# Kernel tuning notes

Hardware: AMD Instinct MI355X
Metric: run time of the kernel (lower is better)

The kernel has to match this reference:

```python
import jax, jax.numpy as jnp
import numpy as np

L, H, P = 32768, 256, 256
DT_MIN, DT_MAX = 0.001, 0.1


def setup_inputs() -> dict:
    key = jax.random.key(0)
    ks = jax.random.split(key, 7)
    signal = jax.random.normal(ks[0], (L, H), jnp.float32)
    # stable HiPPO-like init: negative real part, random imaginary part
    lam_re = -(0.1 + 0.4 * jax.random.uniform(ks[1], (P,), jnp.float32))
    lam_im = jax.random.normal(ks[2], (P,), jnp.float32)
    Lambda_ri = jnp.stack([lam_re, lam_im], axis=-1)            # (P, 2)
    B_ri = jax.random.normal(ks[3], (P, H, 2), jnp.float32) / np.float32(np.sqrt(H))
    C_ri = jax.random.normal(ks[4], (H, P, 2), jnp.float32) / np.float32(np.sqrt(P))
    D = jax.random.uniform(ks[5], (H,), jnp.float32)
    log_step = jnp.log(DT_MIN + (DT_MAX - DT_MIN) * jax.random.uniform(ks[6], (P,), jnp.float32))
    return {"signal": signal, "Lambda_ri": Lambda_ri, "B_ri": B_ri,
            "C_ri": C_ri, "D": D, "log_step": log_step}


def reference(signal, Lambda_ri, B_ri, C_ri, D, log_step):
    # --- get_BC_tilde (bcInit='dense'): B stored real (P,H,2) -> complex ---
    Lambda = jax.lax.complex(Lambda_ri[..., 0], Lambda_ri[..., 1])   # (P,)
    B_tilde = jax.lax.complex(B_ri[..., 0], B_ri[..., 1])            # (P, H)
    C_tilde = jax.lax.complex(C_ri[..., 0], C_ri[..., 1])            # (H, P)

    # --- discretize_zoh ---
    step = jnp.exp(log_step)                                          # (P,) step_scale = 1.0
    Lambda_bar = jnp.exp(Lambda * step)                               # (P,) complex
    B_bar = ((Lambda_bar - 1.0) / Lambda)[:, None] * B_tilde          # (P, H) complex

    # --- apply_ssm: Bu_elements = vmap(u -> B_bar @ u) over time ---
    Bu = signal.astype(Lambda_bar.dtype) @ B_bar.T                    # (L, P) complex
    Lam = jnp.broadcast_to(Lambda_bar, Bu.shape)                      # (L, P)

    def binop(qi, qj):
        A_i, Bu_i = qi
        A_j, Bu_j = qj
        return (A_j * A_i, Bu_j + A_j * Bu_i)

    _, xs = jax.lax.associative_scan(binop, (Lam, Bu), axis=0)        # (L, P)

    # y = Re(C_tilde @ x) + D * u, vectorized over time
    y = jnp.real(xs @ C_tilde.T) + D * signal                         # (L, H)
    return y
```

## Files before the change

kernel.cpp:

```cpp
#include <hip/hip_runtime.h>
#include <math.h>

constexpr int L = 32768;
constexpr int H = 256;
constexpr int P = 256;
constexpr int T = 64;
constexpr int NC = L / T;
constexpr int N1 = 2 * P;
constexpr int LDE = 132;

typedef __attribute__((ext_vector_type(8))) short short8;
typedef __attribute__((ext_vector_type(4))) float f32x4;

__device__ __forceinline__ unsigned f2bf(float f) {
  unsigned u = __float_as_uint(f);
  return (u + 0x7FFFu + ((u >> 16) & 1u)) >> 16;
}
__device__ __forceinline__ float bf_lo(unsigned u) { return __uint_as_float(u << 16); }
__device__ __forceinline__ float bf_hi(unsigned u) { return __uint_as_float(u & 0xFFFF0000u); }

__device__ __forceinline__ void gload_lds16(const unsigned short* g, unsigned short* l) {
  __builtin_amdgcn_global_load_lds(
      (const __attribute__((address_space(1))) unsigned int*)(g),
      (__attribute__((address_space(3))) unsigned int*)(l), 16, 0, 0);
}

__device__ __forceinline__ void lambda_bar_of(const float* __restrict__ lam,
                                              const float* __restrict__ lstep,
                                              int p, float& lbr, float& lbi) {
  float lr = lam[2 * p], li = lam[2 * p + 1];
  float st = expf(lstep[p]);
  float ea = expf(lr * st);
  lbr = ea * cosf(li * st);
  lbi = ea * sinf(li * st);
}

__global__ __launch_bounds__(256) void k_prep(const float* __restrict__ lam,
                                              const float* __restrict__ lstep,
                                              const float* __restrict__ Bri,
                                              const float* __restrict__ Cri,
                                              unsigned short* __restrict__ Bcat,
                                              unsigned short* __restrict__ Ccat,
                                              float* __restrict__ powr,
                                              float* __restrict__ powi) {
  int idx = blockIdx.x * 256 + threadIdx.x;
  if (idx < N1 * H) {
    int n = idx >> 8, k = idx & 255;
    int p = n >> 1, comp = n & 1;
    float lr = lam[2 * p], li = lam[2 * p + 1];
    float st = expf(lstep[p]);
    float ea = expf(lr * st);
    float lbr = ea * cosf(li * st), lbi = ea * sinf(li * st);
    float inv = 1.0f / (lr * lr + li * li);
    float nr = lbr - 1.0f;
    float fr = (nr * lr + lbi * li) * inv;
    float fi = (lbi * lr - nr * li) * inv;
    float br = Bri[2 * (p * H + k)], bi = Bri[2 * (p * H + k) + 1];
    float v = (comp == 0) ? (fr * br - fi * bi) : (fr * bi + fi * br);
    Bcat[idx] = (unsigned short)f2bf(v);
  } else if (idx < 2 * N1 * H) {
    int j = idx - N1 * H;
    int h = j >> 9, k2 = j & 511;
    int p = k2 >> 1;
    float v = ((k2 & 1) == 0) ? Cri[2 * (h * P + p)] : -Cri[2 * (h * P + p) + 1];
    Ccat[j] = (unsigned short)f2bf(v);
  } else {
    int r = idx - 2 * N1 * H;
    int t = r >> 8, p = r & 255;
    float lr = lam[2 * p], li = lam[2 * p + 1];
    float st = expf(lstep[p]);
    float e = (float)(t + 1);
    float er = expf(e * lr * st);
    powr[r] = er * cosf(e * li * st);
    powi[r] = er * sinf(e * li * st);
  }
}

__global__ __launch_bounds__(256) void k_gemm1s(const float* __restrict__ sig,
                                                const unsigned short* __restrict__ Bcat,
                                                const float* __restrict__ lam,
                                                const float* __restrict__ lstep,
                                                unsigned short* __restrict__ Xl,
                                                float* __restrict__ Sr,
                                                float* __restrict__ Si) {
  constexpr int K = 256;
  __shared__ __align__(16) float sEpi[128 * LDE];
  unsigned short* sA = (unsigned short*)sEpi;
  unsigned short* sB = sA + 128 * 32;
  const int tid = threadIdx.x;
  const int lane = tid & 63;
  const int wave = tid >> 6;
  const int wr = (wave >> 1) * 64, wc = (wave & 1) * 64;
  const int m0 = blockIdx.x * 128, n0 = blockIdx.y * 128;
  const int r0 = tid >> 2;
  const int q0 = (tid & 3) * 8;
  const int frow = lane & 15, fk = (lane >> 4) * 8;
  f32x4 acc[4][4];
#pragma unroll
  for (int i = 0; i < 4; i++)
#pragma unroll
    for (int j = 0; j < 4; j++) acc[i][j] = (f32x4){0.f, 0.f, 0.f, 0.f};

  for (int k0 = 0; k0 < K; k0 += 32) {
    float4 a[2][2];
#pragma unroll
    for (int u = 0; u < 2; u++) {
      int row = r0 + u * 64;
      const float* src = sig + (size_t)(m0 + row) * K + k0 + q0;
      a[u][0] = *(const float4*)(src);
      a[u][1] = *(const float4*)(src + 4);
    }
    if (k0) __syncthreads();
    gload_lds16(Bcat + (size_t)(n0 + r0) * K + k0 + q0, sB + tid * 8);
    gload_lds16(Bcat + (size_t)(n0 + 64 + r0) * K + k0 + q0, sB + 2048 + tid * 8);
#pragma unroll
    for (int u = 0; u < 2; u++) {
      int row = r0 + u * 64;
      uint4 w;
      w.x = f2bf(a[u][0].x) | (f2bf(a[u][0].y) << 16);
      w.y = f2bf(a[u][0].z) | (f2bf(a[u][0].w) << 16);
      w.z = f2bf(a[u][1].x) | (f2bf(a[u][1].y) << 16);
      w.w = f2bf(a[u][1].z) | (f2bf(a[u][1].w) << 16);
      *(uint4*)(sA + row * 32 + q0) = w;
    }
    __syncthreads();
    short8 af[4], bfr[4];
#pragma unroll
    for (int i = 0; i < 4; i++) af[i] = *(const short8*)(sA + (wr + i * 16 + frow) * 32 + fk);
#pragma unroll
    for (int j = 0; j < 4; j++) bfr[j] = *(const short8*)(sB + (wc + j * 16 + frow) * 32 + fk);
#pragma unroll
    for (int i = 0; i < 4; i++)
#pragma unroll
      for (int j = 0; j < 4; j++)
        acc[i][j] = __builtin_amdgcn_mfma_f32_16x16x32_bf16(af[i], bfr[j], acc[i][j], 0, 0, 0);
  }

  __syncthreads();
  const int crow = wr + (lane >> 4) * 4, ccol = wc + (lane & 15);
#pragma unroll
  for (int i = 0; i < 4; i++)
#pragma unroll
    for (int j = 0; j < 4; j++)
#pragma unroll
      for (int g = 0; g < 4; g++)
        sEpi[(crow + i * 16 + g) * LDE + ccol + j * 16] = acc[i][j][g];
  __syncthreads();

  if (tid < 128) {
    const int pl = tid & 63;
    const int half = tid >> 6;
    const int c = blockIdx.x * 2 + half;
    const int gp = (n0 >> 1) + pl;
    float lbr, lbi;
    lambda_bar_of(lam, lstep, gp, lbr, lbi);
    float xr = 0.f, xi = 0.f;
    const float* e = sEpi + (half * 64) * LDE + 2 * pl;
    const size_t gbase = (size_t)(m0 + half * 64) * N1 + n0 + 2 * pl;
    for (int tb = 0; tb < T; tb += 8) {
      float2 v[8];
#pragma unroll
      for (int u = 0; u < 8; u++) v[u] = *(const float2*)(e + (tb + u) * LDE);
      unsigned ov[8];
#pragma unroll
      for (int u = 0; u < 8; u++) {
        float nr = fmaf(lbr, xr, fmaf(-lbi, xi, v[u].x));
        float ni = fmaf(lbr, xi, fmaf(lbi, xr, v[u].y));
        xr = nr; xi = ni;
        ov[u] = f2bf(xr) | (f2bf(xi) << 16);
      }
#pragma unroll
      for (int u = 0; u < 8; u++)
        *(unsigned*)(Xl + gbase + (size_t)(tb + u) * N1) = ov[u];
    }
    Sr[c * P + gp] = xr;
    Si[c * P + gp] = xi;
  }
}

__global__ __launch_bounds__(256) void k_carry(const float* __restrict__ lam,
                                               const float* __restrict__ lstep,
                                               const float* __restrict__ Sr,
                                               const float* __restrict__ Si,
                                               float* __restrict__ car, float* __restrict__ cai) {
  const int p = threadIdx.x;
  float lr = lam[2 * p], li = lam[2 * p + 1];
  float st = expf(lstep[p]);
  float ea = expf((float)T * lr * st);
  float lTr = ea * cosf((float)T * li * st);
  float lTi = ea * sinf((float)T * li * st);
  float cr = 0.f, ci = 0.f;
  for (int c0 = 0; c0 < NC; c0 += 16) {
    float vr[16], vi[16];
#pragma unroll
    for (int u = 0; u < 16; u++) {
      vr[u] = Sr[(c0 + u) * P + p];
      vi[u] = Si[(c0 + u) * P + p];
    }
#pragma unroll
    for (int u = 0; u < 16; u++) {
      car[(c0 + u) * P + p] = cr;
      cai[(c0 + u) * P + p] = ci;
      float nr = fmaf(lTr, cr, fmaf(-lTi, ci, vr[u]));
      float ni = fmaf(lTr, ci, fmaf(lTi, cr, vi[u]));
      cr = nr; ci = ni;
    }
  }
}

__global__ __launch_bounds__(256) void k_gemm2f(const unsigned short* __restrict__ Xl,
                                                const unsigned short* __restrict__ Ccat,
                                                const float* __restrict__ powr,
                                                const float* __restrict__ powi,
                                                const float* __restrict__ car,
                                                const float* __restrict__ cai,
                                                const float* __restrict__ sig,
                                                const float* __restrict__ Dv,
                                                float* __restrict__ out) {
  constexpr int K = 512;
  __shared__ __align__(16) unsigned short sA[128 * 32];
  __shared__ __align__(16) unsigned short sB[128 * 32];
  const int tid = threadIdx.x;
  const int lane = tid & 63;
  const int wave = tid >> 6;
  const int wr = (wave >> 1) * 64, wc = (wave & 1) * 64;
  const int m0 = blockIdx.x * 128, n0 = blockIdx.y * 128;
  const int bx2 = blockIdx.x * 2;
  const int r0 = tid >> 2;
  const int q0 = (tid & 3) * 8;
  const int frow = lane & 15, fk = (lane >> 4) * 8;
  f32x4 acc[4][4];
#pragma unroll
  for (int i = 0; i < 4; i++)
#pragma unroll
    for (int j = 0; j < 4; j++) acc[i][j] = (f32x4){0.f, 0.f, 0.f, 0.f};

  for (int k0 = 0; k0 < K; k0 += 32) {
    uint4 xa[2];
    float4 pr4[2], pi4[2], cr4[2], ci4[2];
#pragma unroll
    for (int u = 0; u < 2; u++) {
      int row = r0 + u * 64;
      int t = row & 63;
      int c = bx2 + (row >> 6);
      int p0 = (k0 + q0) >> 1;
      xa[u] = *(const uint4*)(Xl + (size_t)(m0 + row) * K + k0 + q0);
      pr4[u] = *(const float4*)(powr + t * P + p0);
      pi4[u] = *(const float4*)(powi + t * P + p0);
      cr4[u] = *(const float4*)(car + c * P + p0);
      ci4[u] = *(const float4*)(cai + c * P + p0);
    }
    if (k0) __syncthreads();
    gload_lds16(Ccat + (size_t)(n0 + r0) * K + k0 + q0, sB + tid * 8);
    gload_lds16(Ccat + (size_t)(n0 + 64 + r0) * K + k0 + q0, sB + 2048 + tid * 8);
#pragma unroll
    for (int u = 0; u < 2; u++) {
      int row = r0 + u * 64;
      float pr[4] = {pr4[u].x, pr4[u].y, pr4[u].z, pr4[u].w};
      float pi_[4] = {pi4[u].x, pi4[u].y, pi4[u].z, pi4[u].w};
      float cr[4] = {cr4[u].x, cr4[u].y, cr4[u].z, cr4[u].w};
      float ci_[4] = {ci4[u].x, ci4[u].y, ci4[u].z, ci4[u].w};
      unsigned xw[4] = {xa[u].x, xa[u].y, xa[u].z, xa[u].w};
      uint4 w;
      unsigned wo[4];
#pragma unroll
      for (int j = 0; j < 4; j++) {
        float xgr = bf_lo(xw[j]) + (pr[j] * cr[j] - pi_[j] * ci_[j]);
        float xgi = bf_hi(xw[j]) + (pr[j] * ci_[j] + pi_[j] * cr[j]);
        wo[j] = f2bf(xgr) | (f2bf(xgi) << 16);
      }
      w.x = wo[0]; w.y = wo[1]; w.z = wo[2]; w.w = wo[3];
      *(uint4*)(sA + row * 32 + q0) = w;
    }
    __syncthreads();
    short8 af[4], bfr[4];
#pragma unroll
    for (int i = 0; i < 4; i++) af[i] = *(const short8*)(sA + (wr + i * 16 + frow) * 32 + fk);
#pragma unroll
    for (int j = 0; j < 4; j++) bfr[j] = *(const short8*)(sB + (wc + j * 16 + frow) * 32 + fk);
#pragma unroll
    for (int i = 0; i < 4; i++)
#pragma unroll
      for (int j = 0; j < 4; j++)
        acc[i][j] = __builtin_amdgcn_mfma_f32_16x16x32_bf16(af[i], bfr[j], acc[i][j], 0, 0, 0);
  }

  const int crow = wr + (lane >> 4) * 4, ccol = wc + (lane & 15);
  float dcol[4];
#pragma unroll
  for (int j = 0; j < 4; j++) dcol[j] = Dv[n0 + ccol + j * 16];
#pragma unroll
  for (int i = 0; i < 4; i++)
#pragma unroll
    for (int j = 0; j < 4; j++) {
      int col = n0 + ccol + j * 16;
#pragma unroll
      for (int g = 0; g < 4; g++) {
        int row = m0 + crow + i * 16 + g;
        out[(size_t)row * H + col] = acc[i][j][g] + dcol[j] * sig[(size_t)row * H + col];
      }
    }
}

extern "C" void kernel_launch(void* const* d_in, const int* in_sizes, int n_in,
                              void* d_out, int out_size, void* d_ws, size_t ws_size,
                              hipStream_t stream) {
  const float* sig = (const float*)d_in[0];
  const float* lam = (const float*)d_in[1];
  const float* Bri = (const float*)d_in[2];
  const float* Cri = (const float*)d_in[3];
  const float* Dv  = (const float*)d_in[4];
  const float* lst = (const float*)d_in[5];
  float* out = (float*)d_out;

  unsigned short* Bcat = (unsigned short*)d_ws;
  unsigned short* Ccat = Bcat + (size_t)N1 * H;
  unsigned short* Xl   = Ccat + (size_t)H * N1;
  float* powr = (float*)(Xl + (size_t)L * N1);
  float* powi = powr + T * P;
  float* Sr   = powi + T * P;
  float* Si   = Sr + NC * P;
  float* car  = Si + NC * P;
  float* cai  = car + NC * P;

  k_prep<<<(2 * N1 * H + T * P) / 256, 256, 0, stream>>>(lam, lst, Bri, Cri,
                                                         Bcat, Ccat, powr, powi);
  dim3 g1(L / 128, N1 / 128);
  k_gemm1s<<<g1, 256, 0, stream>>>(sig, Bcat, lam, lst, Xl, Sr, Si);
  k_carry<<<1, 256, 0, stream>>>(lam, lst, Sr, Si, car, cai);
  dim3 g2(L / 128, H / 128);
  k_gemm2f<<<g2, 256, 0, stream>>>(Xl, Ccat, powr, powi, car, cai, sig, Dv, out);
}
```

Before: 175.0 us.

## Double-buffer both GEMM main loops and parallelize chunk carry scan across blocks

Both GEMM kernels now use double-buffered LDS tiles. The next A tile is converted and the next B tile is issued through global_load_lds while MFMAs run on the current buffers. The A tile also gets a padded stride (40) to cut LDS bank conflicts. In the first GEMM, the scan epilogue is staged in two 64-row halves so the LDS footprint shrinks. The serial single-block 512-step carry recurrence becomes a per-state block that uses a wave-level shuffle scan with precomputed Lambda^(8T) powers, removing a long latency-bound serial pass. The trade-offs are more registers for prefetched tiles and slightly different floating-point ordering in the carry.

After: 153.8 us. 1.14x faster.

```diff
diff --git a/kernel.cpp b/kernel.cpp
--- a/kernel.cpp
+++ b/kernel.cpp
@@ -7,7 +7,8 @@
 constexpr int T = 64;
 constexpr int NC = L / T;
 constexpr int N1 = 2 * P;
-constexpr int LDE = 132;
+constexpr int LDA = 40;
+constexpr int LDEP = 130;
 
 typedef __attribute__((ext_vector_type(8))) short short8;
 typedef __attribute__((ext_vector_type(4))) float f32x4;
@@ -83,17 +84,18 @@
                                                 unsigned short* __restrict__ Xl,
                                                 float* __restrict__ Sr,
                                                 float* __restrict__ Si) {
-  constexpr int K = 256;
-  __shared__ __align__(16) float sEpi[128 * LDE];
-  unsigned short* sA = (unsigned short*)sEpi;
-  unsigned short* sB = sA + 128 * 32;
+  constexpr int K = 256, NIT = K / 32;
+  __shared__ __align__(16) char smem[36864];
+  unsigned short* sA[2] = {(unsigned short*)smem, (unsigned short*)smem + 5120};
+  unsigned short* sB[2] = {(unsigned short*)smem + 10240, (unsigned short*)smem + 14336};
+  float* sEpi = (float*)smem;
   const int tid = threadIdx.x;
   const int lane = tid & 63;
   const int wave = tid >> 6;
   const int wr = (wave >> 1) * 64, wc = (wave & 1) * 64;
   const int m0 = blockIdx.x * 128, n0 = blockIdx.y * 128;
-  const int r0 = tid >> 2;
-  const int q0 = (tid & 3) * 8;
+  const int ar = tid >> 1, aq = (tid & 1) * 16;
+  const int br = tid >> 2, bq = (tid & 3) * 8;
   const int frow = lane & 15, fk = (lane >> 4) * 8;
   f32x4 acc[4][4];
 #pragma unroll
@@ -101,110 +103,144 @@
 #pragma unroll
     for (int j = 0; j < 4; j++) acc[i][j] = (f32x4){0.f, 0.f, 0.f, 0.f};
 
-  for (int k0 = 0; k0 < K; k0 += 32) {
-    float4 a[2][2];
-#pragma unroll
-    for (int u = 0; u < 2; u++) {
-      int row = r0 + u * 64;
-      const float* src = sig + (size_t)(m0 + row) * K + k0 + q0;
-      a[u][0] = *(const float4*)(src);
-      a[u][1] = *(const float4*)(src + 4);
-    }
-    if (k0) __syncthreads();
-    gload_lds16(Bcat + (size_t)(n0 + r0) * K + k0 + q0, sB + tid * 8);
-    gload_lds16(Bcat + (size_t)(n0 + 64 + r0) * K + k0 + q0, sB + 2048 + tid * 8);
-#pragma unroll
-    for (int u = 0; u < 2; u++) {
-      int row = r0 + u * 64;
-      uint4 w;
-      w.x = f2bf(a[u][0].x) | (f2bf(a[u][0].y) << 16);
-      w.y = f2bf(a[u][0].z) | (f2bf(a[u][0].w) << 16);
-      w.z = f2bf(a[u][1].x) | (f2bf(a[u][1].y) << 16);
-      w.w = f2bf(a[u][1].z) | (f2bf(a[u][1].w) << 16);
-      *(uint4*)(sA + row * 32 + q0) = w;
-    }
+  float4 aR[4];
+  const float* abase = sig + (size_t)(m0 + ar) * K + aq;
+#define LOAD_A(k0) { const float* s_ = abase + (k0); \
+    aR[0] = *(const float4*)(s_); aR[1] = *(const float4*)(s_ + 4); \
+    aR[2] = *(const float4*)(s_ + 8); aR[3] = *(const float4*)(s_ + 12); }
+#define WRITE_A(buf) { uint4 w0, w1; \
+    w0.x = f2bf(aR[0].x) | (f2bf(aR[0].y) << 16); w0.y = f2bf(aR[0].z) | (f2bf(aR[0].w) << 16); \
+    w0.z = f2bf(aR[1].x) | (f2bf(aR[1].y) << 16); w0.w = f2bf(aR[1].z) | (f2bf(aR[1].w) << 16); \
+    w1.x = f2bf(aR[2].x) | (f2bf(aR[2].y) << 16); w1.y = f2bf(aR[2].z) | (f2bf(aR[2].w) << 16); \
+    w1.z = f2bf(aR[3].x) | (f2bf(aR[3].y) << 16); w1.w = f2bf(aR[3].z) | (f2bf(aR[3].w) << 16); \
+    *(uint4*)(sA[buf] + ar * LDA + aq) = w0; *(uint4*)(sA[buf] + ar * LDA + aq + 8) = w1; }
+#define ISSUE_B(k0, buf) { \
+    gload_lds16(Bcat + (size_t)(n0 + br) * K + (k0) + bq, sB[buf] + tid * 8); \
+    gload_lds16(Bcat + (size_t)(n0 + 64 + br) * K + (k0) + bq, sB[buf] + 2048 + tid * 8); }
+
+  LOAD_A(0);
+  ISSUE_B(0, 0);
+  WRITE_A(0);
+  LOAD_A(32);
+  __syncthreads();
+#pragma unroll
+  for (int it = 0; it < NIT; it++) {
+    const int cur = it & 1, nxt = cur ^ 1;
+    if (it + 1 < NIT) {
+      WRITE_A(nxt);
+      ISSUE_B((it + 1) * 32, nxt);
+      if (it + 2 < NIT) LOAD_A((it + 2) * 32);
+    }
+    short8 af[4], bf[4];
+#pragma unroll
+    for (int i = 0; i < 4; i++) af[i] = *(const short8*)(sA[cur] + (wr + i * 16 + frow) * LDA + fk);
+#pragma unroll
+    for (int j = 0; j < 4; j++) bf[j] = *(const short8*)(sB[cur] + (wc + j * 16 + frow) * 32 + fk);
+#pragma unroll
+    for (int i = 0; i < 4; i++)
+#pragma unroll
+      for (int j = 0; j < 4; j++)
+        acc[i][j] = __builtin_amdgcn_mfma_f32_16x16x32_bf16(af[i], bf[j], acc[i][j], 0, 0, 0);
     __syncthreads();
-    short8 af[4], bfr[4];
-#pragma unroll
-    for (int i = 0; i < 4; i++) af[i] = *(const short8*)(sA + (wr + i * 16 + frow) * 32 + fk);
-#pragma unroll
-    for (int j = 0; j < 4; j++) bfr[j] = *(const short8*)(sB + (wc + j * 16 + frow) * 32 + fk);
-#pragma unroll
-    for (int i = 0; i < 4; i++)
-#pragma unroll
-      for (int j = 0; j < 4; j++)
-        acc[i][j] = __builtin_amdgcn_mfma_f32_16x16x32_bf16(af[i], bfr[j], acc[i][j], 0, 0, 0);
-  }
-
-  __syncthreads();
-  const int crow = wr + (lane >> 4) * 4, ccol = wc + (lane & 15);
-#pragma unroll
-  for (int i = 0; i < 4; i++)
-#pragma unroll
-    for (int j = 0; j < 4; j++)
-#pragma unroll
-      for (int g = 0; g < 4; g++)
-        sEpi[(crow + i * 16 + g) * LDE + ccol + j * 16] = acc[i][j][g];
-  __syncthreads();
-
-  if (tid < 128) {
-    const int pl = tid & 63;
-    const int half = tid >> 6;
-    const int c = blockIdx.x * 2 + half;
-    const int gp = (n0 >> 1) + pl;
-    float lbr, lbi;
-    lambda_bar_of(lam, lstep, gp, lbr, lbi);
-    float xr = 0.f, xi = 0.f;
-    const float* e = sEpi + (half * 64) * LDE + 2 * pl;
-    const size_t gbase = (size_t)(m0 + half * 64) * N1 + n0 + 2 * pl;
-    for (int tb = 0; tb < T; tb += 8) {
-      float2 v[8];
-#pragma unroll
-      for (int u = 0; u < 8; u++) v[u] = *(const float2*)(e + (tb + u) * LDE);
-      unsigned ov[8];
-#pragma unroll
-      for (int u = 0; u < 8; u++) {
-        float nr = fmaf(lbr, xr, fmaf(-lbi, xi, v[u].x));
-        float ni = fmaf(lbr, xi, fmaf(lbi, xr, v[u].y));
-        xr = nr; xi = ni;
-        ov[u] = f2bf(xr) | (f2bf(xi) << 16);
+  }
+
+  const int crow = (lane >> 4) * 4, ccol = wc + (lane & 15);
+#pragma unroll
+  for (int half = 0; half < 2; half++) {
+    if ((wave >> 1) == half) {
+#pragma unroll
+      for (int i = 0; i < 4; i++)
+#pragma unroll
+        for (int j = 0; j < 4; j++)
+#pragma unroll
+          for (int g = 0; g < 4; g++)
+            sEpi[(crow + i * 16 + g) * LDEP + ccol + j * 16] = acc[i][j][g];
+    }
+    __syncthreads();
+    if (tid < 64) {
+      const int pl = tid;
+      const int gp = (n0 >> 1) + pl;
+      const int c = blockIdx.x * 2 + half;
+      float lbr, lbi;
+      lambda_bar_of(lam, lstep, gp, lbr, lbi);
+      float xr = 0.f, xi = 0.f;
+      const float* e = sEpi + 2 * pl;
+      const size_t gbase = (size_t)(m0 + half * 64) * N1 + n0 + 2 * pl;
+      for (int tb = 0; tb < T; tb += 8) {
+        float2 v[8];
+#pragma unroll
+        for (int u = 0; u < 8; u++) v[u] = *(const float2*)(e + (tb + u) * LDEP);
+        unsigned ov[8];
+#pragma unroll
+        for (int u = 0; u < 8; u++) {
+          float nr = fmaf(lbr, xr, fmaf(-lbi, xi, v[u].x));
+          float ni = fmaf(lbr, xi, fmaf(lbi, xr, v[u].y));
+          xr = nr; xi = ni;
+          ov[u] = f2bf(xr) | (f2bf(xi) << 16);
+        }
+#pragma unroll
+        for (int u = 0; u < 8; u++)
+          *(unsigned*)(Xl + gbase + (size_t)(tb + u) * N1) = ov[u];
       }
-#pragma unroll
-      for (int u = 0; u < 8; u++)
-        *(unsigned*)(Xl + gbase + (size_t)(tb + u) * N1) = ov[u];
-    }
-    Sr[c * P + gp] = xr;
-    Si[c * P + gp] = xi;
-  }
-}
-
-__global__ __launch_bounds__(256) void k_carry(const float* __restrict__ lam,
+      Sr[c * P + gp] = xr;
+      Si[c * P + gp] = xi;
+    }
+    __syncthreads();
+  }
+#undef LOAD_A
+#undef WRITE_A
+#undef ISSUE_B
+}
+
+__global__ __launch_bounds__(64) void k_carry2(const float* __restrict__ lam,
                                                const float* __restrict__ lstep,
                                                const float* __restrict__ Sr,
                                                const float* __restrict__ Si,
                                                float* __restrict__ car, float* __restrict__ cai) {
-  const int p = threadIdx.x;
+  const int p = blockIdx.x;
+  const int t = threadIdx.x;
   float lr = lam[2 * p], li = lam[2 * p + 1];
   float st = expf(lstep[p]);
-  float ea = expf((float)T * lr * st);
-  float lTr = ea * cosf((float)T * li * st);
-  float lTi = ea * sinf((float)T * li * st);
-  float cr = 0.f, ci = 0.f;
-  for (int c0 = 0; c0 < NC; c0 += 16) {
-    float vr[16], vi[16];
-#pragma unroll
-    for (int u = 0; u < 16; u++) {
-      vr[u] = Sr[(c0 + u) * P + p];
-      vi[u] = Si[(c0 + u) * P + p];
-    }
-#pragma unroll
-    for (int u = 0; u < 16; u++) {
-      car[(c0 + u) * P + p] = cr;
-      cai[(c0 + u) * P + p] = ci;
-      float nr = fmaf(lTr, cr, fmaf(-lTi, ci, vr[u]));
-      float ni = fmaf(lTr, ci, fmaf(lTi, cr, vi[u]));
-      cr = nr; ci = ni;
-    }
+  float eT = expf((float)T * lr * st);
+  float lTr = eT * cosf((float)T * li * st);
+  float lTi = eT * sinf((float)T * li * st);
+  float vr[8], vi[8];
+#pragma unroll
+  for (int u = 0; u < 8; u++) {
+    vr[u] = Sr[(t * 8 + u) * P + p];
+    vi[u] = Si[(t * 8 + u) * P + p];
+  }
+  float Br = 0.f, Bi = 0.f;
+#pragma unroll
+  for (int u = 0; u < 8; u++) {
+    float nr = fmaf(lTr, Br, fmaf(-lTi, Bi, vr[u]));
+    float ni = fmaf(lTr, Bi, fmaf(lTi, Br, vi[u]));
+    Br = nr; Bi = ni;
+  }
+  float e8 = expf(8.0f * (float)T * lr * st);
+  float Ar = e8 * cosf(8.0f * (float)T * li * st);
+  float Ai = e8 * sinf(8.0f * (float)T * li * st);
+#pragma unroll
+  for (int d = 1; d < 64; d <<= 1) {
+    float Aor = __shfl_up(Ar, d), Aoi = __shfl_up(Ai, d);
+    float Bor = __shfl_up(Br, d), Boi = __shfl_up(Bi, d);
+    if (t >= d) {
+      float nBr = Ar * Bor - Ai * Boi + Br;
+      float nBi = Ar * Boi + Ai * Bor + Bi;
+      float nAr = Aor * Ar - Aoi * Ai;
+      float nAi = Aor * Ai + Aoi * Ar;
+      Br = nBr; Bi = nBi; Ar = nAr; Ai = nAi;
+    }
+  }
+  float cr = __shfl_up(Br, 1), ci = __shfl_up(Bi, 1);
+  if (t == 0) { cr = 0.f; ci = 0.f; }
+#pragma unroll
+  for (int u = 0; u < 8; u++) {
+    car[(t * 8 + u) * P + p] = cr;
+    cai[(t * 8 + u) * P + p] = ci;
+    float nr = fmaf(lTr, cr, fmaf(-lTi, ci, vr[u]));
+    float ni = fmaf(lTr, ci, fmaf(lTi, cr, vi[u]));
+    cr = nr; ci = ni;
   }
 }
 
@@ -217,17 +253,19 @@
                                                 const float* __restrict__ sig,
                                                 const float* __restrict__ Dv,
                                                 float* __restrict__ out) {
-  constexpr int K = 512;
-  __shared__ __align__(16) unsigned short sA[128 * 32];
-  __shared__ __align__(16) unsigned short sB[128 * 32];
+  constexpr int K = 512, NIT = K / 32;
+  __shared__ __align__(16) char smem[36864];
+  unsigned short* sA[2] = {(unsigned short*)smem, (unsigned short*)smem + 5120};
+  unsigned short* sB[2] = {(unsigned short*)smem + 10240, (unsigned short*)smem + 14336};
   const int tid = threadIdx.x;
   const int lane = tid & 63;
   const int wave = tid >> 6;
   const int wr = (wave >> 1) * 64, wc = (wave & 1) * 64;
   const int m0 = blockIdx.x * 128, n0 = blockIdx.y * 128;
-  const int bx2 = blockIdx.x * 2;
-  const int r0 = tid >> 2;
-  const int q0 = (tid & 3) * 8;
+  const int ar = tid >> 1, aq = (tid & 1) * 16;
+  const int t_ = ar & 63;
+  const int cc = blockIdx.x * 2 + (ar >> 6);
+  const int br = tid >> 2, bq = (tid & 3) * 8;
   const int frow = lane & 15, fk = (lane >> 4) * 8;
   f32x4 acc[4][4];
 #pragma unroll
@@ -235,54 +273,62 @@
 #pragma unroll
     for (int j = 0; j < 4; j++) acc[i][j] = (f32x4){0.f, 0.f, 0.f, 0.f};
 
-  for (int k0 = 0; k0 < K; k0 += 32) {
-    uint4 xa[2];
-    float4 pr4[2], pi4[2], cr4[2], ci4[2];
-#pragma unroll
-    for (int u = 0; u < 2; u++) {
-      int row = r0 + u * 64;
-      int t = row & 63;
-      int c = bx2 + (row >> 6);
-      int p0 = (k0 + q0) >> 1;
-      xa[u] = *(const uint4*)(Xl + (size_t)(m0 + row) * K + k0 + q0);
-      pr4[u] = *(const float4*)(powr + t * P + p0);
-      pi4[u] = *(const float4*)(powi + t * P + p0);
-      cr4[u] = *(const float4*)(car + c * P + p0);
-      ci4[u] = *(const float4*)(cai + c * P + p0);
-    }
-    if (k0) __syncthreads();
-    gload_lds16(Ccat + (size_t)(n0 + r0) * K + k0 + q0, sB + tid * 8);
-    gload_lds16(Ccat + (size_t)(n0 + 64 + r0) * K + k0 + q0, sB + 2048 + tid * 8);
-#pragma unroll
-    for (int u = 0; u < 2; u++) {
-      int row = r0 + u * 64;
-      float pr[4] = {pr4[u].x, pr4[u].y, pr4[u].z, pr4[u].w};
-      float pi_[4] = {pi4[u].x, pi4[u].y, pi4[u].z, pi4[u].w};
-      float cr[4] = {cr4[u].x, cr4[u].y, cr4[u].z, cr4[u].w};
-      float ci_[4] = {ci4[u].x, ci4[u].y, ci4[u].z, ci4[u].w};
-      unsigned xw[4] = {xa[u].x, xa[u].y, xa[u].z, xa[u].w};
-      uint4 w;
-      unsigned wo[4];
-#pragma unroll
-      for (int j = 0; j < 4; j++) {
-        float xgr = bf_lo(xw[j]) + (pr[j] * cr[j] - pi_[j] * ci_[j]);
-        float xgi = bf_hi(xw[j]) + (pr[j] * ci_[j] + pi_[j] * cr[j]);
-        wo[j] = f2bf(xgr) | (f2bf(xgi) << 16);
-      }
-      w.x = wo[0]; w.y = wo[1]; w.z = wo[2]; w.w = wo[3];
-      *(uint4*)(sA + row * 32 + q0) = w;
-    }
+  uint4 x0, x1;
+  float4 pr0, pr1, pi0, pi1, cr0, cr1, ci0, ci1;
+  const unsigned short* xbase = Xl + (size_t)(m0 + ar) * N1 + aq;
+  const float* prb = powr + t_ * P;
+  const float* pib = powi + t_ * P;
+  const float* crb = car + cc * P;
+  const float* cib = cai + cc * P;
+#define LOAD_A2(k0) { int p0_ = ((k0) >> 1) + (tid & 1) * 8; \
+    x0 = *(const uint4*)(xbase + (k0)); x1 = *(const uint4*)(xbase + (k0) + 8); \
+    pr0 = *(const float4*)(prb + p0_); pr1 = *(const float4*)(prb + p0_ + 4); \
+    pi0 = *(const float4*)(pib + p0_); pi1 = *(const float4*)(pib + p0_ + 4); \
+    cr0 = *(const float4*)(crb + p0_); cr1 = *(const float4*)(crb + p0_ + 4); \
+    ci0 = *(const float4*)(cib + p0_); ci1 = *(const float4*)(cib + p0_ + 4); }
+#define WRITE_A2(buf) { \
+    unsigned xw[8] = {x0.x, x0.y, x0.z, x0.w, x1.x, x1.y, x1.z, x1.w}; \
+    float pr_[8] = {pr0.x, pr0.y, pr0.z, pr0.w, pr1.x, pr1.y, pr1.z, pr1.w}; \
+    float pi_[8] = {pi0.x, pi0.y, pi0.z, pi0.w, pi1.x, pi1.y, pi1.z, pi1.w}; \
+    float cr_[8] = {cr0.x, cr0.y, cr0.z, cr0.w, cr1.x, cr1.y, cr1.z, cr1.w}; \
+    float ci_[8] = {ci0.x, ci0.y, ci0.z, ci0.w, ci1.x, ci1.y, ci1.z, ci1.w}; \
+    unsigned wo[8]; \
+    _Pragma("unroll") for (int j_ = 0; j_ < 8; j_++) { \
+      float xgr = bf_lo(xw[j_]) + (pr_[j_] * cr_[j_] - pi_[j_] * ci_[j_]); \
+      float xgi = bf_hi(xw[j_]) + (pr_[j_] * ci_[j_] + pi_[j_] * cr_[j_]); \
+      wo[j_] = f2bf(xgr) | (f2bf(xgi) << 16); } \
+    uint4 w0, w1; \
+    w0.x = wo[0]; w0.y = wo[1]; w0.z = wo[2]; w0.w = wo[3]; \
+    w1.x = wo[4]; w1.y = wo[5]; w1.z = wo[6]; w1.w = wo[7]; \
+    *(uint4*)(sA[buf] + ar * LDA + aq) = w0; *(uint4*)(sA[buf] + ar * LDA + aq + 8) = w1; }
+#define ISSUE_B2(k0, buf) { \
+    gload_lds16(Ccat + (size_t)(n0 + br) * K + (k0) + bq, sB[buf] + tid * 8); \
+    gload_lds16(Ccat + (size_t)(n0 + 64 + br) * K + (k0) + bq, sB[buf] + 2048 + tid * 8); }
+
+  LOAD_A2(0);
+  ISSUE_B2(0, 0);
+  WRITE_A2(0);
+  LOAD_A2(32);
+  __syncthreads();
+#pragma unroll
+  for (int it = 0; it < NIT; it++) {
+    const int cur = it & 1, nxt = cur ^ 1;
+    if (it + 1 < NIT) {
+      WRITE_A2(nxt);
+      ISSUE_B2((it + 1) * 32, nxt);
+      if (it + 2 < NIT) LOAD_A2((it + 2) * 32);
+    }
+    short8 af[4], bf[4];
+#pragma unroll
+    for (int i = 0; i < 4; i++) af[i] = *(const short8*)(sA[cur] + (wr + i * 16 + frow) * LDA + fk);
+#pragma unroll
+    for (int j = 0; j < 4; j++) bf[j] = *(const short8*)(sB[cur] + (wc + j * 16 + frow) * 32 + fk);
+#pragma unroll
+    for (int i = 0; i < 4; i++)
+#pragma unroll
+      for (int j = 0; j < 4; j++)
+        acc[i][j] = __builtin_amdgcn_mfma_f32_16x16x32_bf16(af[i], bf[j], acc[i][j], 0, 0, 0);
     __syncthreads();
-    short8 af[4], bfr[4];
-#pragma unroll
-    for (int i = 0; i < 4; i++) af[i] = *(const short8*)(sA + (wr + i * 16 + frow) * 32 + fk);
-#pragma unroll
-    for (int j = 0; j < 4; j++) bfr[j] = *(const short8*)(sB + (wc + j * 16 + frow) * 32 + fk);
-#pragma unroll
-    for (int i = 0; i < 4; i++)
-#pragma unroll
-      for (int j = 0; j < 4; j++)
-        acc[i][j] = __builtin_amdgcn_mfma_f32_16x16x32_bf16(af[i], bfr[j], acc[i][j], 0, 0, 0);
   }
 
   const int crow = wr + (lane >> 4) * 4, ccol = wc + (lane & 15);
@@ -300,6 +346,9 @@
         out[(size_t)row * H + col] = acc[i][j][g] + dcol[j] * sig[(size_t)row * H + col];
       }
     }
+#undef LOAD_A2
+#undef WRITE_A2
+#undef ISSUE_B2
 }
 
 extern "C" void kernel_launch(void* const* d_in, const int* in_sizes, int n_in,
@@ -327,7 +376,7 @@
                                                          Bcat, Ccat, powr, powi);
   dim3 g1(L / 128, N1 / 128);
   k_gemm1s<<<g1, 256, 0, stream>>>(sig, Bcat, lam, lst, Xl, Sr, Si);
-  k_carry<<<1, 256, 0, stream>>>(lam, lst, Sr, Si, car, cai);
+  k_carry2<<<NC / 2, 64, 0, stream>>>(lam, lst, Sr, Si, car, cai);
   dim3 g2(L / 128, H / 128);
   k_gemm2f<<<g2, 256, 0, stream>>>(Xl, Ccat, powr, powi, car, cai, sig, Dv, out);
 }
```
